# Kernel optimization log

Hardware: AMD Instinct MI355X
Metric: run time of the kernel (lower is better)

Reference implementation:

```python
import jax, jax.numpy as jnp
import numpy as np
import math

K = 30   # neighbors
T = 9    # num_kernel

def sparsemax(z):
    # sparsemax along last axis
    zs = jnp.sort(z, axis=-1)[..., ::-1]
    rng = jnp.arange(1, z.shape[-1] + 1, dtype=z.dtype)
    cs = jnp.cumsum(zs, axis=-1)
    support = (1.0 + rng * zs) > cs
    kz = jnp.sum(support, axis=-1, keepdims=True)
    tau = (jnp.take_along_axis(cs, kz - 1, axis=-1) - 1.0) / kz.astype(z.dtype)
    return jnp.maximum(z - tau, 0.0)

def bn(x, g, b, axes, eps=1e-5):
    # batch-norm (training-mode batch stats), channel axis = 1
    m = jnp.mean(x, axes, keepdims=True)
    v = jnp.var(x, axes, keepdims=True)
    sh = [1] * x.ndim; sh[1] = -1
    return (x - m) / jnp.sqrt(v + eps) * g.reshape(sh) + b.reshape(sh)

def _forward(x, B_ff, mlp_W, permx, W1, b1, S1, W2, b2, S2, W3, b3, S3, W4, b4, S4,
             W5, g5, be5, L1, g6, be6, L2, bL2, g7, be7, L3, bL3):
    Bsz, _, N = x.shape
    pts = jnp.transpose(x, (0, 2, 1))                      # [B,N,3]
    # knn (DGCNN-style): negative squared distance, top-k (self first)
    xx = jnp.sum(pts * pts, -1)                            # [B,N]
    inner = jnp.einsum('bnc,bmc->bnm', pts, pts)
    negd = 2.0 * inner - xx[:, :, None] - xx[:, None, :]
    _, idx = jax.lax.top_k(negd, K)                        # [B,N,K] int32
    gather = jax.vmap(lambda f, i: f[i])                   # [B,N,F],[B,N,K]->[B,N,K,F]
    # Fourier features -> sparsemax basis weights -> per-point permatrix
    ng = gather(pts, idx)                                  # [B,N,K,3]
    xrep = jnp.broadcast_to(ng[:, :, :1, :], ng.shape)     # self repeated
    rel = ng - xrep
    sq = jnp.sum(rel * rel, -1, keepdims=True)
    dist = jnp.where(sq > 0, jnp.sqrt(jnp.where(sq > 0, sq, 1.0)), 0.0)  # safe norm
    feats = jnp.concatenate([xrep, rel, dist], -1).reshape(Bsz, N, 7 * K)
    ff = (2.0 * math.pi) * (feats @ B_ff)                  # [B,N,32]
    ff = jnp.concatenate([jnp.sin(ff), jnp.cos(ff)], -1)   # [B,N,64]
    w = sparsemax(ff @ mlp_W)                              # [B,N,16]
    P = jnp.einsum('bni,ikt->bnkt', w, permx)              # [B,N,K,T]

    def paiconv(f, W, b, S):  # f: [B,Cin,N]
        ft = jnp.transpose(f, (0, 2, 1))                   # [B,N,Cin]
        nb = gather(ft, idx)                               # [B,N,K,Cin]
        agg = jnp.einsum('bnkc,bnkt->bntc', nb, P).reshape(Bsz, N, -1)
        out = agg @ W + b + ft @ S                         # [B,N,Cout]
        return jnp.transpose(out, (0, 2, 1))

    gelu = lambda a: jax.nn.gelu(a, approximate=False)
    x1 = gelu(paiconv(x,  W1, b1, S1))
    x2 = gelu(paiconv(x1, W2, b2, S2))
    x3 = gelu(paiconv(x2, W3, b3, S3))
    x4 = gelu(paiconv(x3, W4, b4, S4))
    f = jnp.concatenate([x1, x2, x3, x4], 1)               # [B,512,N]
    f = jnp.einsum('bcn,ce->ben', f, W5)                   # conv5 (1x1)
    f = gelu(bn(f, g5, be5, (0, 2)))
    h = jnp.concatenate([jnp.max(f, -1), jnp.mean(f, -1)], -1)  # [B,2048]
    h = gelu(bn(h @ L1, g6, be6, (0,)))
    h = gelu(bn(h @ L2 + bL2, g7, be7, (0,)))
    return h @ L3 + bL3


def setup_inputs() -> dict:
    key = jax.random.key(0)
    ks = jax.random.split(key, 20)
    rn = lambda k_, sh, s=1.0: jax.random.normal(k_, sh, dtype=jnp.float32) * s
    B, N = 16, 1024
    inp = {}
    inp['x'] = rn(ks[0], (B, 3, N))
    inp['B_ff'] = rn(ks[1], (7 * K, 32))
    inp['mlp_W'] = rn(ks[2], (64, 16), 0.125)
    inp['permx'] = rn(ks[3], (16, K, T), 0.1)
    dims = [(3, 64), (64, 64), (64, 128), (128, 256)]
    for i, (ci, co) in enumerate(dims, 1):
        inp['W%d' % i] = rn(ks[3 + i], (T * ci, co), 1.0 / float(np.sqrt(T * ci)))
        inp['b%d' % i] = jnp.zeros((co,), jnp.float32)
        inp['S%d' % i] = rn(ks[7 + i], (ci, co), 1.0 / float(np.sqrt(ci)))
    inp['W5'] = rn(ks[12], (512, 1024), 1.0 / float(np.sqrt(512)))
    inp['g5'] = jnp.ones((1024,), jnp.float32); inp['be5'] = jnp.zeros((1024,), jnp.float32)
    inp['L1'] = rn(ks[13], (2048, 512), 1.0 / float(np.sqrt(2048)))
    inp['g6'] = jnp.ones((512,), jnp.float32); inp['be6'] = jnp.zeros((512,), jnp.float32)
    inp['L2'] = rn(ks[14], (512, 256), 1.0 / float(np.sqrt(512))); inp['bL2'] = jnp.zeros((256,), jnp.float32)
    inp['g7'] = jnp.ones((256,), jnp.float32); inp['be7'] = jnp.zeros((256,), jnp.float32)
    inp['L3'] = rn(ks[15], (256, 40), 1.0 / float(np.sqrt(256))); inp['bL3'] = jnp.zeros((40,), jnp.float32)
    return inp


def reference(x, B_ff, mlp_W, permx, W1, b1, S1, W2, b2, S2, W3, b3, S3, W4, b4, S4,
              W5, g5, be5, L1, g6, be6, L2, bL2, g7, be7, L3, bL3):
    return _forward(x, B_ff, mlp_W, permx, W1, b1, S1, W2, b2, S2, W3, b3, S3, W4, b4, S4,
                    W5, g5, be5, L1, g6, be6, L2, bL2, g7, be7, L3, bL3)
```

## Files before the change

kernel.cpp:

```cpp
#include <hip/hip_runtime.h>
#include <hip/hip_bf16.h>
#include <cstddef>

#define BSZ 16
#define NPT 1024
#define KNN 30
#define TKR 9
#define FLT_BIG 3.402823466e+38f

typedef unsigned short u16;
typedef __attribute__((ext_vector_type(8))) u16 u16x8;
typedef __attribute__((ext_vector_type(4))) float f32x4;

__device__ __forceinline__ float gelu_f(float x) {
    return 0.5f * x * (1.0f + erff(x * 0.7071067811865476f));
}

__device__ __forceinline__ u16 bf16_rne(float a) {
    unsigned u = __float_as_uint(a);
    u += 0x7FFFu + ((u >> 16) & 1u);
    return (u16)(u >> 16);
}
__device__ __forceinline__ float bf16_tof(u16 h) {
    return __uint_as_float(((unsigned)h) << 16);
}
__device__ __forceinline__ void split_bf16(float a, u16& h, u16& l) {
    h = bf16_rne(a);
    float r = a - bf16_tof(h);
    l = bf16_rne(r);
}

__device__ __forceinline__ size_t pack_off(int row, int k, int npanels_row) {
    return (size_t)((k >> 5) * npanels_row + (row >> 7)) * 4096
         + (size_t)(((k >> 3) & 3) * 1024 + (row & 127) * 8 + (k & 7));
}

__global__ __launch_bounds__(256) void prep_all(
    const float* __restrict__ x, float* __restrict__ pts,
    const float* __restrict__ W1, const float* __restrict__ S1, float* __restrict__ wz1,
    const float* __restrict__ W2, const float* __restrict__ S2, float* __restrict__ wz2,
    const float* __restrict__ W3, const float* __restrict__ S3, float* __restrict__ wz3,
    const float* __restrict__ W4, const float* __restrict__ S4,
    u16* __restrict__ w4tH, u16* __restrict__ w4tL) {
    int layer = blockIdx.y;
    int t = blockIdx.x * 256 + threadIdx.x;
    if (layer == 0) {
        if (t >= BSZ * NPT) return;
        int b = t >> 10, n = t & 1023;
        const float* xp = x + (size_t)b * 3 * NPT;
        pts[t * 3 + 0] = xp[n];
        pts[t * 3 + 1] = xp[NPT + n];
        pts[t * 3 + 2] = xp[2 * NPT + n];
        return;
    }
    if (layer == 4) {
        if (t >= 1280 * 256) return;
        int k = t >> 8, n = t & 255;
        float v = (k < 1152) ? W4[(size_t)k * 256 + n] : S4[(size_t)(k - 1152) * 256 + n];
        u16 h, l;
        split_bf16(v, h, l);
        size_t off = pack_off(n, k, 2);
        w4tH[off] = h;
        w4tL[off] = l;
        return;
    }
    const float *W, *S; float* WZ; int KW, KS, N, kpad;
    if (layer == 1)      { W = W1; S = S1; WZ = wz1; KW = 27;   KS = 3;   N = 64;  kpad = 32;  }
    else if (layer == 2) { W = W2; S = S2; WZ = wz2; KW = 576;  KS = 64;  N = 64;  kpad = 640; }
    else                 { W = W3; S = S3; WZ = wz3; KW = 576;  KS = 64;  N = 128; kpad = 640; }
    if (t >= kpad * N) return;
    int k = t / N, n = t - k * N;
    float v = 0.0f;
    if (k < KW) v = W[(size_t)k * N + n];
    else if (k < KW + KS) v = S[(size_t)(k - KW) * N + n];
    WZ[t] = v;
}

__global__ __launch_bounds__(256) void knn_basis_kernel(
    const float* __restrict__ pts, const float* __restrict__ B_ff,
    const float* __restrict__ mlp_W, const float* __restrict__ permx,
    int* __restrict__ idx, float* __restrict__ P) {
    __shared__ float npt[4][KNN * 3];
    __shared__ float feats[4][7 * KNN];
    __shared__ float sc[4][64];
    __shared__ float zl[4][16];
    __shared__ float w[4][16];
    __shared__ float sZs[4][16];
    __shared__ float sCs[4][16];
    __shared__ int sIds[4][KNN];
    int tid = threadIdx.x;
    int wave = tid >> 6, lane = tid & 63;
    int bn_ = blockIdx.x * 4 + wave;
    int b = bn_ >> 10;

    {
        double px = (double)pts[(size_t)bn_ * 3 + 0];
        double py = (double)pts[(size_t)bn_ * 3 + 1];
        double pz = (double)pts[(size_t)bn_ * 3 + 2];
        double xn = px * px + py * py + pz * pz;
        const float* pb = pts + (size_t)(b << 10) * 3;
        int base = lane * 16;
        unsigned mono[16];
        #pragma unroll
        for (int j = 0; j < 16; j++) {
            int m = base + j;
            double qx = (double)pb[m * 3 + 0];
            double qy = (double)pb[m * 3 + 1];
            double qz = (double)pb[m * 3 + 2];
            double inner = px * qx + py * qy + pz * qz;
            double xm = qx * qx + qy * qy + qz * qz;
            double cd = 2.0 * inner - xn - xm;
            float cf = (float)cd;
            unsigned bb = __float_as_uint(cf);
            mono[j] = (bb & 0x80000000u) ? ~bb : (bb | 0x80000000u);
        }
        unsigned alive = 0xFFFFu;
        unsigned c1v = 0u, c2v = 0u;
        int c1j = 0, c2j = 0;
        #pragma unroll
        for (int j = 0; j < 16; j++) {
            unsigned v = mono[j];
            if (v > c1v) { c2v = c1v; c2j = c1j; c1v = v; c1j = j; }
            else if (v > c2v) { c2v = v; c2j = j; }
        }
        bool have2 = true;
        for (int it = 0; it < KNN; it++) {
            unsigned m = c1v;
            #pragma unroll
            for (int s = 1; s < 64; s <<= 1) {
                unsigned ov = (unsigned)__shfl_xor((int)m, s, 64);
                m = (ov > m) ? ov : m;
            }
            unsigned long long ball = __ballot(c1v == m);
            int wlan = (int)__builtin_ctzll(ball);
            int jw = __shfl(c1j, wlan, 64);
            int bi = (wlan << 4) + jw;
            if (lane == it) sIds[wave][it] = bi;
            if (lane == wlan) {
                alive &= ~(1u << c1j);
                if (have2) {
                    c1v = c2v; c1j = c2j; have2 = false;
                } else {
                    unsigned a1 = 0u, a2 = 0u;
                    int j1 = 0, j2 = 0;
                    #pragma unroll
                    for (int j = 0; j < 16; j++) {
                        unsigned v = ((alive >> j) & 1u) ? mono[j] : 0u;
                        if (v > a1) { a2 = a1; j2 = j1; a1 = v; j1 = j; }
                        else if (v > a2) { a2 = v; j2 = j; }
                    }
                    c1v = a1; c1j = j1; c2v = a2; c2j = j2;
                    have2 = true;
                }
            }
        }
        __builtin_amdgcn_wave_barrier();
        if (lane < KNN) idx[(size_t)bn_ * KNN + lane] = sIds[wave][lane];
    }
    __syncthreads();

    if (lane < KNN) {
        int m = sIds[wave][lane];
        const float* q = pts + ((size_t)(b << 10) + m) * 3;
        npt[wave][lane * 3 + 0] = q[0];
        npt[wave][lane * 3 + 1] = q[1];
        npt[wave][lane * 3 + 2] = q[2];
    }
    __syncthreads();
    if (lane < KNN) {
        float sx = npt[wave][0], sy = npt[wave][1], sz = npt[wave][2];
        float rx = npt[wave][lane * 3 + 0] - sx;
        float ry = npt[wave][lane * 3 + 1] - sy;
        float rz = npt[wave][lane * 3 + 2] - sz;
        float sq = rx * rx + ry * ry + rz * rz;
        float dist = (sq > 0.0f) ? sqrtf(sq) : 0.0f;
        feats[wave][lane * 7 + 0] = sx;
        feats[wave][lane * 7 + 1] = sy;
        feats[wave][lane * 7 + 2] = sz;
        feats[wave][lane * 7 + 3] = rx;
        feats[wave][lane * 7 + 4] = ry;
        feats[wave][lane * 7 + 5] = rz;
        feats[wave][lane * 7 + 6] = dist;
    }
    __syncthreads();
    {
        int j = lane & 31;
        int half = lane >> 5;
        int i0 = half * 105;
        float acc = 0.0f;
        for (int i = i0; i < i0 + 105; i++) acc += feats[wave][i] * B_ff[i * 32 + j];
        acc += __shfl_xor(acc, 32, 64);
        if (half == 0) {
            float ffv = 6.283185307179586f * acc;
            sc[wave][j] = sinf(ffv);
            sc[wave][j + 32] = cosf(ffv);
        }
    }
    __syncthreads();
    {
        int j = lane & 15;
        int h = lane >> 4;
        float acc = 0.0f;
        for (int i = 16 * h; i < 16 * h + 16; i++) acc += sc[wave][i] * mlp_W[i * 16 + j];
        acc += __shfl_xor(acc, 16, 64);
        acc += __shfl_xor(acc, 32, 64);
        if (h == 0) zl[wave][j] = acc;
    }
    __syncthreads();
    {
        int l = lane & 15;
        float zv = zl[wave][l];
        int rank = 0;
        #pragma unroll
        for (int j = 0; j < 16; j++) {
            float zj = zl[wave][j];
            rank += (zj > zv || (zj == zv && j < l)) ? 1 : 0;
        }
        if (lane < 16) sZs[wave][rank] = zv;
        __builtin_amdgcn_wave_barrier();
        float cs = 0.0f;
        #pragma unroll
        for (int p = 0; p < 16; p++) {
            float zp = sZs[wave][p];
            cs += (p <= l) ? zp : 0.0f;
        }
        float zsl = sZs[wave][l];
        bool flag = (lane < 16) && (1.0f + (float)(l + 1) * zsl > cs);
        unsigned long long ball = __ballot(flag);
        int cnt = (int)__popcll(ball & 0xFFFFull);
        if (lane < 16) sCs[wave][l] = cs;
        __builtin_amdgcn_wave_barrier();
        float tau = (sCs[wave][cnt - 1] - 1.0f) / (float)cnt;
        if (lane < 16) w[wave][l] = fmaxf(zv - tau, 0.0f);
    }
    __syncthreads();
    float* Pp = P + (size_t)bn_ * (KNN * TKR);
    for (int e = lane; e < KNN * TKR; e += 64) {
        int k = e / TKR, t = e - TKR * k;
        float acc = 0.0f;
        for (int i = 0; i < 16; i++) acc += w[wave][i] * permx[(i * KNN + k) * TKR + t];
        Pp[e] = acc;
    }
}

template <int CIN>
__global__ __launch_bounds__(256) void agg_kernel(
    const float* __restrict__ ft, int ftst,
    const float* __restrict__ P, const int* __restrict__ idx,
    float* __restrict__ Z, int kpad) {
    __shared__ float sP[KNN * TKR];
    __shared__ float sNb[KNN * CIN];
    __shared__ int sIdx[KNN];
    int bn_ = blockIdx.x;
    int b = bn_ >> 10;
    int tid = threadIdx.x;
    if (tid < KNN) sIdx[tid] = idx[(size_t)bn_ * KNN + tid];
    for (int e = tid; e < KNN * TKR; e += 256) sP[e] = P[(size_t)bn_ * (KNN * TKR) + e];
    __syncthreads();
    for (int e = tid; e < KNN * CIN; e += 256) {
        int k = e / CIN, c = e - k * CIN;
        sNb[e] = ft[((size_t)(b << 10) + sIdx[k]) * ftst + c];
    }
    __syncthreads();
    float* zp = Z + (size_t)bn_ * kpad;
    const int KW = TKR * CIN;
    for (int e = tid; e < kpad; e += 256) {
        float v;
        if (e < KW) {
            int t = e / CIN, c = e - t * CIN;
            float acc = 0.0f;
            #pragma unroll
            for (int k = 0; k < KNN; k++) acc += sNb[k * CIN + c] * sP[k * TKR + t];
            v = acc;
        } else if (e < KW + CIN) {
            v = ft[(size_t)bn_ * ftst + (e - KW)];
        } else {
            v = 0.0f;
        }
        zp[e] = v;
    }
}

template <int CIN>
__global__ __launch_bounds__(256) void agg_v_kernel(
    const float* __restrict__ ft, int ftst,
    const float* __restrict__ P, const int* __restrict__ idx,
    float* __restrict__ Z, int kpad) {
    __shared__ float sP[KNN * TKR];
    __shared__ float sNb[KNN * CIN];
    __shared__ int sIdx[KNN];
    constexpr int C4 = CIN / 4;
    int bn_ = blockIdx.x;
    int b = bn_ >> 10;
    int tid = threadIdx.x;
    if (tid < KNN) sIdx[tid] = idx[(size_t)bn_ * KNN + tid];
    for (int e = tid; e < KNN * TKR; e += 256) sP[e] = P[(size_t)bn_ * (KNN * TKR) + e];
    __syncthreads();
    for (int e = tid; e < KNN * C4; e += 256) {
        int k = e / C4, c4 = (e - k * C4) * 4;
        *(float4*)&sNb[k * CIN + c4] =
            *(const float4*)&ft[((size_t)(b << 10) + sIdx[k]) * ftst + c4];
    }
    __syncthreads();
    float* zp = Z + (size_t)bn_ * kpad;
    const int KW = TKR * CIN;
    for (int e = tid; e < (kpad >> 2); e += 256) {
        int c0 = e * 4;
        float4 v;
        if (c0 < KW) {
            int t = c0 / CIN, c4 = c0 - t * CIN;
            float4 a = make_float4(0.f, 0.f, 0.f, 0.f);
            #pragma unroll
            for (int k = 0; k < KNN; k++) {
                float p = sP[k * TKR + t];
                float4 nb = *(const float4*)&sNb[k * CIN + c4];
                a.x += nb.x * p; a.y += nb.y * p;
                a.z += nb.z * p; a.w += nb.w * p;
            }
            v = a;
        } else if (c0 < KW + CIN) {
            v = *(const float4*)&ft[(size_t)bn_ * ftst + (c0 - KW)];
        } else {
            v = make_float4(0.f, 0.f, 0.f, 0.f);
        }
        *(float4*)&zp[c0] = v;
    }
}

template <int CIN>
__global__ __launch_bounds__(256) void agg_v_split_kernel(
    const float* __restrict__ ft, int ftst,
    const float* __restrict__ P, const int* __restrict__ idx,
    u16* __restrict__ ZH, u16* __restrict__ ZL, int kpad) {
    __shared__ float sP[KNN * TKR];
    __shared__ float sNb[KNN * CIN];
    __shared__ int sIdx[KNN];
    constexpr int C4 = CIN / 4;
    int bn_ = blockIdx.x;
    int b = bn_ >> 10;
    int tid = threadIdx.x;
    if (tid < KNN) sIdx[tid] = idx[(size_t)bn_ * KNN + tid];
    for (int e = tid; e < KNN * TKR; e += 256) sP[e] = P[(size_t)bn_ * (KNN * TKR) + e];
    __syncthreads();
    for (int e = tid; e < KNN * C4; e += 256) {
        int k = e / C4, c4 = (e - k * C4) * 4;
        *(float4*)&sNb[k * CIN + c4] =
            *(const float4*)&ft[((size_t)(b << 10) + sIdx[k]) * ftst + c4];
    }
    __syncthreads();
    const int KW = TKR * CIN;
    for (int e = tid; e < (kpad >> 2); e += 256) {
        int c0 = e * 4;
        float4 v;
        if (c0 < KW) {
            int t = c0 / CIN, c4 = c0 - t * CIN;
            float4 a = make_float4(0.f, 0.f, 0.f, 0.f);
            #pragma unroll
            for (int k = 0; k < KNN; k++) {
                float p = sP[k * TKR + t];
                float4 nb = *(const float4*)&sNb[k * CIN + c4];
                a.x += nb.x * p; a.y += nb.y * p;
                a.z += nb.z * p; a.w += nb.w * p;
            }
            v = a;
        } else if (c0 < KW + CIN) {
            v = *(const float4*)&ft[(size_t)bn_ * ftst + (c0 - KW)];
        } else {
            v = make_float4(0.f, 0.f, 0.f, 0.f);
        }
        u16 h[4], l[4];
        split_bf16(v.x, h[0], l[0]);
        split_bf16(v.y, h[1], l[1]);
        split_bf16(v.z, h[2], l[2]);
        split_bf16(v.w, h[3], l[3]);
        uint2 hv, lv;
        hv.x = (unsigned)h[0] | ((unsigned)h[1] << 16);
        hv.y = (unsigned)h[2] | ((unsigned)h[3] << 16);
        lv.x = (unsigned)l[0] | ((unsigned)l[1] << 16);
        lv.y = (unsigned)l[2] | ((unsigned)l[3] << 16);
        size_t off = pack_off(bn_, c0, 128);
        *(uint2*)&ZH[off] = hv;
        *(uint2*)&ZL[off] = lv;
    }
}

template <bool GELU, bool HASBIAS>
__global__ __launch_bounds__(256) void gemm_f32_64db(
    const float* __restrict__ A, int lda,
    const float* __restrict__ B, int ldb, int K,
    const float* __restrict__ bias,
    float* __restrict__ C, int ldc) {
    __shared__ float As[2][16][64];
    __shared__ float Bs[2][16][64];
    int tid = threadIdx.x;
    int tx = tid & 15, ty = tid >> 4;
    int m0 = blockIdx.y * 64, n0 = blockIdx.x * 64;
    float acc[4][4];
    #pragma unroll
    for (int i = 0; i < 4; i++)
        #pragma unroll
        for (int j = 0; j < 4; j++) acc[i][j] = 0.0f;

    int ar = tid >> 2, ac0 = (tid & 3) * 4;
    const float* aptr = A + (size_t)(m0 + ar) * lda + ac0;
    int br = tid >> 4, bc = (tid & 15) * 4;
    const float* bptr = B + (size_t)br * ldb + n0 + bc;

    float4 pa = *(const float4*)(aptr);
    float4 pb = *(const float4*)(bptr);
    As[0][ac0 + 0][ar] = pa.x; As[0][ac0 + 1][ar] = pa.y;
    As[0][ac0 + 2][ar] = pa.z; As[0][ac0 + 3][ar] = pa.w;
    *(float4*)&Bs[0][br][bc] = pb;
    __syncthreads();

    int nk = K >> 4;
    for (int t = 0; t < nk; t++) {
        int buf = t & 1;
        bool more = (t + 1) < nk;
        if (more) {
            int k0 = (t + 1) << 4;
            pa = *(const float4*)(aptr + k0);
            pb = *(const float4*)(bptr + (size_t)k0 * ldb);
        }
        #pragma unroll
        for (int kk = 0; kk < 16; kk++) {
            float av[4], bv[4];
            *(float4*)&av[0] = *(const float4*)&As[buf][kk][ty * 4];
            *(float4*)&bv[0] = *(const float4*)&Bs[buf][kk][tx * 4];
            #pragma unroll
            for (int i = 0; i < 4; i++)
                #pragma unroll
                for (int j = 0; j < 4; j++) acc[i][j] += av[i] * bv[j];
        }
        if (more) {
            int nb = 1 - buf;
            As[nb][ac0 + 0][ar] = pa.x; As[nb][ac0 + 1][ar] = pa.y;
            As[nb][ac0 + 2][ar] = pa.z; As[nb][ac0 + 3][ar] = pa.w;
            *(float4*)&Bs[nb][br][bc] = pb;
        }
        __syncthreads();
    }
    #pragma unroll
    for (int i = 0; i < 4; i++) {
        int r = m0 + ty * 4 + i;
        int c = n0 + tx * 4;
        float v[4];
        #pragma unroll
        for (int j = 0; j < 4; j++) {
            float t = acc[i][j];
            if (HASBIAS) t += bias[c + j];
            if (GELU) t = gelu_f(t);
            v[j] = t;
        }
        *(float4*)(C + (size_t)r * ldc + c) = *(float4*)v;
    }
}

__global__ __launch_bounds__(256) void convert_split(
    const float* __restrict__ feat, u16* __restrict__ fH, u16* __restrict__ fL,
    const float* __restrict__ W5, u16* __restrict__ wH, u16* __restrict__ wL) {
    int t = blockIdx.x * 256 + threadIdx.x;
    if (blockIdx.y == 0) {
        int base = t << 3;
        int row = base >> 9, k0 = base & 511;
        float4 a = *(const float4*)&feat[base];
        float4 b = *(const float4*)&feat[base + 4];
        float v[8] = {a.x, a.y, a.z, a.w, b.x, b.y, b.z, b.w};
        u16 h[8], l[8];
        #pragma unroll
        for (int i = 0; i < 8; i++) split_bf16(v[i], h[i], l[i]);
        uint4 hv, lv;
        hv.x = (unsigned)h[0] | ((unsigned)h[1] << 16);
        hv.y = (unsigned)h[2] | ((unsigned)h[3] << 16);
        hv.z = (unsigned)h[4] | ((unsigned)h[5] << 16);
        hv.w = (unsigned)h[6] | ((unsigned)h[7] << 16);
        lv.x = (unsigned)l[0] | ((unsigned)l[1] << 16);
        lv.y = (unsigned)l[2] | ((unsigned)l[3] << 16);
        lv.z = (unsigned)l[4] | ((unsigned)l[5] << 16);
        lv.w = (unsigned)l[6] | ((unsigned)l[7] << 16);
        size_t off = pack_off(row, k0, 128);
        *(uint4*)&fH[off] = hv;
        *(uint4*)&fL[off] = lv;
    } else {
        if (t >= 512 * 1024) return;
        int n = t >> 9, k = t & 511;
        u16 h, l;
        split_bf16(W5[(size_t)k * 1024 + n], h, l);
        size_t off = pack_off(n, k, 8);
        wH[off] = h; wL[off] = l;
    }
}

template <bool STATS, bool GELU, bool HASBIAS>
__global__ __launch_bounds__(256) void mfma_bf16x3(
    const u16* __restrict__ fH, const u16* __restrict__ fL,
    const u16* __restrict__ wH, const u16* __restrict__ wL,
    int K, const float* __restrict__ bias,
    float* __restrict__ C, int ldc,
    float* __restrict__ partS, float* __restrict__ partQ) {
    __shared__ __align__(16) u16 lds[2][16384];
    int tid = threadIdx.x;
    int lane = tid & 63, wave = tid >> 6;
    int wr = wave >> 1, wc = wave & 1;
    int kg = lane >> 4, r = lane & 15;

    int nwg = gridDim.x * gridDim.y;
    int hw = blockIdx.y * gridDim.x + blockIdx.x;
    int logical = (hw & 7) * (nwg >> 3) + (hw >> 3);
    int nb = logical % gridDim.x;
    int mb = logical / gridDim.x;
    int m0 = mb << 7, n0 = nb << 7;
    int nmp = gridDim.y;
    int nnp = gridDim.x;

    const u16* src = (wave == 0) ? fH : (wave == 1) ? fL
                   : (wave == 2) ? wH : wL;

    f32x4 acc[4][4];
    #pragma unroll
    for (int i = 0; i < 4; i++)
        #pragma unroll
        for (int j = 0; j < 4; j++) {
            acc[i][j][0] = 0.0f; acc[i][j][1] = 0.0f;
            acc[i][j][2] = 0.0f; acc[i][j][3] = 0.0f;
        }

#define STAGE_K(BUF, TT) {                                                     \
    size_t tb = ((size_t)((wave < 2) ? ((TT) * nmp + mb)                       \
                                     : ((TT) * nnp + nb)) << 12);              \
    _Pragma("unroll")                                                          \
    for (int iw = 0; iw < 8; iw++) {                                           \
        const u16* gp = src + tb + (size_t)(((iw << 6) + lane) << 3);          \
        __builtin_amdgcn_global_load_lds(                                      \
            (const __attribute__((address_space(1))) void*)gp,                 \
            (__attribute__((address_space(3))) void*)&lds[BUF][(wave << 12) + (iw << 9)], \
            16, 0, 0);                                                         \
    } }

    int nk = K >> 5;
    STAGE_K(0, 0);
    __syncthreads();
    for (int t = 0; t < nk; t++) {
        if (t + 1 < nk) STAGE_K((t + 1) & 1, (t + 1));
        const u16* lb = lds[t & 1];
        u16x8 bh[4], bl[4];
        #pragma unroll
        for (int fj = 0; fj < 4; fj++) {
            int bcol = (wc << 6) + (fj << 4) + r;
            bh[fj] = *(const u16x8*)&lb[ 8192 + (((kg << 7) + bcol) << 3)];
            bl[fj] = *(const u16x8*)&lb[12288 + (((kg << 7) + bcol) << 3)];
        }
        #pragma unroll
        for (int fi = 0; fi < 4; fi++) {
            int arow = (wr << 6) + (fi << 4) + r;
            u16x8 ah = *(const u16x8*)&lb[       (((kg << 7) + arow) << 3)];
            u16x8 al = *(const u16x8*)&lb[4096 + (((kg << 7) + arow) << 3)];
            #pragma unroll
            for (int fj = 0; fj < 4; fj++) {
                asm volatile("v_mfma_f32_16x16x32_bf16 %0, %1, %2, %0"
                             : "+v"(acc[fi][fj]) : "v"(ah), "v"(bh[fj]));
                asm volatile("v_mfma_f32_16x16x32_bf16 %0, %1, %2, %0"
                             : "+v"(acc[fi][fj]) : "v"(ah), "v"(bl[fj]));
                asm volatile("v_mfma_f32_16x16x32_bf16 %0, %1, %2, %0"
                             : "+v"(acc[fi][fj]) : "v"(al), "v"(bh[fj]));
            }
        }
        __syncthreads();
    }
#undef STAGE_K

    asm volatile("s_nop 15\n\ts_nop 15" ::: "memory");

    float bvv[4];
    if (HASBIAS) {
        #pragma unroll
        for (int fj = 0; fj < 4; fj++) bvv[fj] = bias[n0 + (wc << 6) + (fj << 4) + r];
    }

    #pragma unroll
    for (int fi = 0; fi < 4; fi++)
        #pragma unroll
        for (int ri = 0; ri < 4; ri++) {
            int row = m0 + (wr << 6) + (fi << 4) + (kg << 2) + ri;
            float* cp = C + (size_t)row * ldc + n0 + (wc << 6) + r;
            #pragma unroll
            for (int fj = 0; fj < 4; fj++) {
                float v = acc[fi][fj][ri];
                if (HASBIAS) v += bvv[fj];
                if (GELU) v = gelu_f(v);
                cp[fj << 4] = v;
            }
        }

    if (STATS) {
        __syncthreads();
        float* sS = (float*)lds;
        float* sQ = sS + 1024;
        int slot = (wr << 2) + kg;
        #pragma unroll
        for (int fj = 0; fj < 4; fj++) {
            float s = 0.0f, q = 0.0f;
            #pragma unroll
            for (int fi = 0; fi < 4; fi++)
                #pragma unroll
                for (int ri = 0; ri < 4; ri++) {
                    float v = acc[fi][fj][ri];
                    s += v; q += v * v;
                }
            int cl = (wc << 6) + (fj << 4) + r;
            sS[slot * 128 + cl] = s;
            sQ[slot * 128 + cl] = q;
        }
        __syncthreads();
        if (tid < 128) {
            float S = 0.0f, Q = 0.0f;
            #pragma unroll
            for (int i = 0; i < 8; i++) { S += sS[i * 128 + tid]; Q += sQ[i * 128 + tid]; }
            partS[(size_t)mb * 1024 + n0 + tid] = S;
            partQ[(size_t)mb * 1024 + n0 + tid] = Q;
        }
    }
}

__global__ __launch_bounds__(256) void stats_reduce(
    const float* __restrict__ partS, const float* __restrict__ partQ,
    const float* __restrict__ g, const float* __restrict__ be,
    float* __restrict__ scaleb, float* __restrict__ shiftb) {
    int e = blockIdx.x * 256 + threadIdx.x;
    if (e >= 1024) return;
    double s = 0.0, q = 0.0;
    for (int mb = 0; mb < 128; mb++) {
        s += (double)partS[(size_t)mb * 1024 + e];
        q += (double)partQ[(size_t)mb * 1024 + e];
    }
    double m = s * (1.0 / 16384.0);
    double v = q * (1.0 / 16384.0) - m * m;
    float sc = g[e] * (float)(1.0 / sqrt(v + 1e-5));
    scaleb[e] = sc;
    shiftb[e] = be[e] - (float)m * sc;
}

__global__ __launch_bounds__(256) void pool_partial(
    const float* __restrict__ f5, const float* __restrict__ scaleb,
    const float* __restrict__ shiftb,
    float* __restrict__ partM, double* __restrict__ partSd) {
    int chunk = blockIdx.x, g = blockIdx.y, b = blockIdx.z;
    int tid = threadIdx.x;
    int lane = tid & 63, nlane = tid >> 6;
    int c0 = (g << 8) + lane * 4;
    float4 sc = *(const float4*)&scaleb[c0];
    float4 sh = *(const float4*)&shiftb[c0];
    float m0 = -FLT_BIG, m1 = -FLT_BIG, m2 = -FLT_BIG, m3 = -FLT_BIG;
    double s0 = 0.0, s1 = 0.0, s2 = 0.0, s3 = 0.0;
    int nend = (chunk + 1) << 6;
    for (int n = (chunk << 6) + nlane; n < nend; n += 4) {
        float4 v = *(const float4*)&f5[((size_t)(b << 10) + n) * 1024 + c0];
        float g0 = gelu_f(v.x * sc.x + sh.x);
        float g1 = gelu_f(v.y * sc.y + sh.y);
        float g2 = gelu_f(v.z * sc.z + sh.z);
        float g3 = gelu_f(v.w * sc.w + sh.w);
        m0 = fmaxf(m0, g0); m1 = fmaxf(m1, g1);
        m2 = fmaxf(m2, g2); m3 = fmaxf(m3, g3);
        s0 += (double)g0; s1 += (double)g1;
        s2 += (double)g2; s3 += (double)g3;
    }
    __shared__ float smax[4][256];
    __shared__ double ssum[4][256];
    *(float4*)&smax[nlane][lane * 4] = make_float4(m0, m1, m2, m3);
    ssum[nlane][lane * 4 + 0] = s0;
    ssum[nlane][lane * 4 + 1] = s1;
    ssum[nlane][lane * 4 + 2] = s2;
    ssum[nlane][lane * 4 + 3] = s3;
    __syncthreads();
    if (nlane == 0) {
        size_t base = ((size_t)((b * 4 + g) * 16 + chunk)) * 256 + lane * 4;
        #pragma unroll
        for (int j = 0; j < 4; j++) {
            float mm = smax[0][lane * 4 + j];
            double ss = ssum[0][lane * 4 + j];
            #pragma unroll
            for (int i = 1; i < 4; i++) {
                mm = fmaxf(mm, smax[i][lane * 4 + j]);
                ss += ssum[i][lane * 4 + j];
            }
            partM[base + j] = mm;
            partSd[base + j] = ss;
        }
    }
}

__global__ __launch_bounds__(256) void pool_finish(
    const float* __restrict__ partM, const double* __restrict__ partSd,
    float* __restrict__ h) {
    int b = blockIdx.x;
    int e0 = threadIdx.x * 4;
    int g = e0 >> 8, cl = e0 & 255;
    float mm[4] = {-FLT_BIG, -FLT_BIG, -FLT_BIG, -FLT_BIG};
    double ss[4] = {0.0, 0.0, 0.0, 0.0};
    for (int chunk = 0; chunk < 16; chunk++) {
        size_t base = ((size_t)((b * 4 + g) * 16 + chunk)) * 256 + cl;
        float4 pm = *(const float4*)&partM[base];
        mm[0] = fmaxf(mm[0], pm.x); mm[1] = fmaxf(mm[1], pm.y);
        mm[2] = fmaxf(mm[2], pm.z); mm[3] = fmaxf(mm[3], pm.w);
        ss[0] += partSd[base + 0]; ss[1] += partSd[base + 1];
        ss[2] += partSd[base + 2]; ss[3] += partSd[base + 3];
    }
    #pragma unroll
    for (int j = 0; j < 4; j++) {
        h[(size_t)b * 2048 + e0 + j] = mm[j];
        h[(size_t)b * 2048 + 1024 + e0 + j] = (float)(ss[j] * (1.0 / 1024.0));
    }
}

__global__ __launch_bounds__(256) void fc_split(
    const float* __restrict__ X, const float* __restrict__ W,
    double* __restrict__ part, int Bn, int In, int Out, int KC) {
    int tid = blockIdx.x * 256 + threadIdx.x;
    if (tid >= Bn * Out * KC) return;
    int chunk = tid / (Bn * Out);
    int r = tid - chunk * (Bn * Out);
    int b = r / Out, j = r - b * Out;
    int len = In / KC;
    int i0 = chunk * len;
    const float* x = X + (size_t)b * In + i0;
    const float* w = W + (size_t)i0 * Out + j;
    double acc = 0.0;
    for (int i = 0; i < len; i++) acc += (double)x[i] * (double)w[(size_t)i * Out];
    part[tid] = acc;
}

__global__ __launch_bounds__(256) void fc_bn_gelu(
    const double* __restrict__ part, const float* __restrict__ bias,
    const float* __restrict__ g, const float* __restrict__ be,
    float* __restrict__ Y, int Out, int KC) {
    int j = blockIdx.x * 256 + threadIdx.x;
    if (j >= Out) return;
    float r[BSZ];
    for (int b = 0; b < BSZ; b++) {
        double acc = bias ? (double)bias[j] : 0.0;
        for (int c = 0; c < KC; c++) acc += part[(size_t)c * (BSZ * Out) + b * Out + j];
        r[b] = (float)acc;
    }
    double m = 0.0;
    for (int b = 0; b < BSZ; b++) m += (double)r[b];
    m /= (double)BSZ;
    double v = 0.0;
    for (int b = 0; b < BSZ; b++) {
        double dd = (double)r[b] - m;
        v += dd * dd;
    }
    v /= (double)BSZ;
    float sc = g[j] * (float)(1.0 / sqrt(v + 1e-5));
    float sh = be[j] - (float)m * sc;
    for (int b = 0; b < BSZ; b++) Y[b * Out + j] = gelu_f(r[b] * sc + sh);
}

__global__ __launch_bounds__(256) void fc_reduce(
    const double* __restrict__ part, const float* __restrict__ bias,
    float* __restrict__ Y, int Bn, int Out, int KC) {
    int r = blockIdx.x * 256 + threadIdx.x;
    if (r >= Bn * Out) return;
    int j = r % Out;
    double acc = bias ? (double)bias[j] : 0.0;
    for (int c = 0; c < KC; c++) acc += part[(size_t)c * (Bn * Out) + r];
    Y[r] = (float)acc;
}

extern "C" void kernel_launch(void* const* d_in, const int* in_sizes, int n_in,
                              void* d_out, int out_size, void* d_ws, size_t ws_size,
                              hipStream_t stream) {
    const float* x     = (const float*)d_in[0];
    const float* B_ff  = (const float*)d_in[1];
    const float* mlp_W = (const float*)d_in[2];
    const float* permx = (const float*)d_in[3];
    const float* W1 = (const float*)d_in[4];
    const float* b1 = (const float*)d_in[5];
    const float* S1 = (const float*)d_in[6];
    const float* W2 = (const float*)d_in[7];
    const float* b2 = (const float*)d_in[8];
    const float* S2 = (const float*)d_in[9];
    const float* W3 = (const float*)d_in[10];
    const float* b3 = (const float*)d_in[11];
    const float* S3 = (const float*)d_in[12];
    const float* W4 = (const float*)d_in[13];
    const float* b4 = (const float*)d_in[14];
    const float* S4 = (const float*)d_in[15];
    const float* W5 = (const float*)d_in[16];
    const float* g5 = (const float*)d_in[17];
    const float* be5 = (const float*)d_in[18];
    const float* L1 = (const float*)d_in[19];
    const float* g6 = (const float*)d_in[20];
    const float* be6 = (const float*)d_in[21];
    const float* L2 = (const float*)d_in[22];
    const float* bL2 = (const float*)d_in[23];
    const float* g7 = (const float*)d_in[24];
    const float* be7 = (const float*)d_in[25];
    const float* L3 = (const float*)d_in[26];
    const float* bL3 = (const float*)d_in[27];
    float* outp = (float*)d_out;

    const int BN = BSZ * NPT;

    float* ws = (float*)d_ws;
    float* pts   = ws;
    int*   idxb  = (int*)(ws + 49152);
    float* Pb    = ws + 540672;
    float* feat  = Pb + 4423680;
    float* Zbig  = feat + 8388608;
    u16*   ZH    = (u16*)Zbig;
    u16*   ZL    = (u16*)(Zbig + 10485760);
    float* f5    = Zbig;
    u16*   featH = (u16*)(Zbig + 16777216);
    float* poolM = Zbig + 16777216;
    double* poolS = (double*)(Zbig + 16777216 + 262144);
    float* w4slot = Zbig + 20971520;
    u16*   w4tH  = (u16*)w4slot;
    u16*   w4tL  = w4tH + 327680;
    float* scb   = w4slot + 327680;
    float* shb   = scb + 1024;
    float* hb    = shb + 1024;
    float* y1    = hb + 32768;
    float* y2    = y1 + 8192;
    float* partC_S = y2 + 4096;
    float* partC_Q = partC_S + 131072;
    double* partF  = (double*)(partC_Q + 131072);
    float* wsend = (float*)(partF + 131072);
    u16* featL = (u16*)ws;
    u16* w5tH  = (u16*)(ws + 4194304);
    u16* w5tL  = (u16*)(ws + 4456448);
    float* wz1   = Zbig + 11010048;
    float* wz2   = wz1 + 2048;
    float* wz3   = wz2 + 40960;
    size_t need_bytes = (size_t)(wsend - ws) * sizeof(float);
    if (ws_size < need_bytes) return;

    prep_all<<<dim3(1280, 5), 256, 0, stream>>>(
        x, pts, W1, S1, wz1, W2, S2, wz2, W3, S3, wz3, W4, S4, w4tH, w4tL);

    knn_basis_kernel<<<BN / 4, 256, 0, stream>>>(pts, B_ff, mlp_W, permx, idxb, Pb);

    agg_kernel<3><<<BN, 256, 0, stream>>>(pts, 3, Pb, idxb, Zbig, 32);
    gemm_f32_64db<true, true><<<dim3(1, 256), 256, 0, stream>>>(
        Zbig, 32, wz1, 64, 32, b1, feat + 0, 512);
    agg_v_kernel<64><<<BN, 256, 0, stream>>>(feat + 0, 512, Pb, idxb, Zbig, 640);
    gemm_f32_64db<true, true><<<dim3(1, 256), 256, 0, stream>>>(
        Zbig, 640, wz2, 64, 640, b2, feat + 64, 512);
    agg_v_kernel<64><<<BN, 256, 0, stream>>>(feat + 64, 512, Pb, idxb, Zbig, 640);
    gemm_f32_64db<true, true><<<dim3(2, 256), 256, 0, stream>>>(
        Zbig, 640, wz3, 128, 640, b3, feat + 128, 512);
    agg_v_split_kernel<128><<<BN, 256, 0, stream>>>(feat + 128, 512, Pb, idxb, ZH, ZL, 1280);
    mfma_bf16x3<false, true, true><<<dim3(2, 128), 256, 0, stream>>>(
        ZH, ZL, w4tH, w4tL, 1280, b4, feat + 256, 512, nullptr, nullptr);

    convert_split<<<dim3(4096, 2), 256, 0, stream>>>(feat, featH, featL, W5, w5tH, w5tL);
    mfma_bf16x3<true, false, false><<<dim3(8, 128), 256, 0, stream>>>(
        featH, featL, w5tH, w5tL, 512, nullptr, f5, 1024, partC_S, partC_Q);

    stats_reduce<<<4, 256, 0, stream>>>(partC_S, partC_Q, g5, be5, scb, shb);
    pool_partial<<<dim3(16, 4, BSZ), 256, 0, stream>>>(f5, scb, shb, poolM, poolS);
    pool_finish<<<BSZ, 256, 0, stream>>>(poolM, poolS, hb);

    fc_split<<<(BSZ * 512 * 16 + 255) / 256, 256, 0, stream>>>(hb, L1, partF, BSZ, 2048, 512, 16);
    fc_bn_gelu<<<2, 256, 0, stream>>>(partF, nullptr, g6, be6, y1, 512, 16);
    fc_split<<<(BSZ * 256 * 8 + 255) / 256, 256, 0, stream>>>(y1, L2, partF, BSZ, 512, 256, 8);
    fc_bn_gelu<<<1, 256, 0, stream>>>(partF, bL2, g7, be7, y2, 256, 8);
    fc_split<<<(BSZ * 40 * 4 + 255) / 256, 256, 0, stream>>>(y2, L3, partF, BSZ, 256, 40, 4);
    fc_reduce<<<(BSZ * 40 + 255) / 256, 256, 0, stream>>>(partF, bL3, outp, BSZ, 40, 4);
}
```

Measured before the change: 743.0 us.

## Process four points per block in split aggregation and coalesce packed bf16 writes

The split aggregation kernel now handles four points per block, one per wavefront. Outputs are staged in shared memory and then written out in the packed tile layout, so each store covers contiguous runs across rows instead of scattered 8-byte writes. The feature-conversion kernel remaps its thread indices the same way, so consecutive threads write consecutive packed offsets. This uses more shared memory per block, which may lower occupancy, and it hardcodes the packed layout arithmetic.

```diff
diff --git a/kernel.cpp b/kernel.cpp
--- a/kernel.cpp
+++ b/kernel.cpp
@@ -327,60 +327,86 @@
     }
 }
 
-template <int CIN>
-__global__ __launch_bounds__(256) void agg_v_split_kernel(
+__global__ __launch_bounds__(256) void agg_v_split4_kernel(
     const float* __restrict__ ft, int ftst,
     const float* __restrict__ P, const int* __restrict__ idx,
-    u16* __restrict__ ZH, u16* __restrict__ ZL, int kpad) {
-    __shared__ float sP[KNN * TKR];
-    __shared__ float sNb[KNN * CIN];
-    __shared__ int sIdx[KNN];
-    constexpr int C4 = CIN / 4;
-    int bn_ = blockIdx.x;
-    int b = bn_ >> 10;
+    u16* __restrict__ ZH, u16* __restrict__ ZL) {
+    __shared__ int   sIdx4[4][KNN];
+    __shared__ float sP4[4][KNN * TKR + 2];
+    __shared__ float sNb4[4][KNN * 128];
+    __shared__ __align__(16) u16 oH[4][640];
+    __shared__ __align__(16) u16 oL[4][640];
     int tid = threadIdx.x;
-    if (tid < KNN) sIdx[tid] = idx[(size_t)bn_ * KNN + tid];
-    for (int e = tid; e < KNN * TKR; e += 256) sP[e] = P[(size_t)bn_ * (KNN * TKR) + e];
-    __syncthreads();
-    for (int e = tid; e < KNN * C4; e += 256) {
-        int k = e / C4, c4 = (e - k * C4) * 4;
-        *(float4*)&sNb[k * CIN + c4] =
-            *(const float4*)&ft[((size_t)(b << 10) + sIdx[k]) * ftst + c4];
-    }
-    __syncthreads();
-    const int KW = TKR * CIN;
-    for (int e = tid; e < (kpad >> 2); e += 256) {
-        int c0 = e * 4;
-        float4 v;
-        if (c0 < KW) {
-            int t = c0 / CIN, c4 = c0 - t * CIN;
-            float4 a = make_float4(0.f, 0.f, 0.f, 0.f);
-            #pragma unroll
-            for (int k = 0; k < KNN; k++) {
-                float p = sP[k * TKR + t];
-                float4 nb = *(const float4*)&sNb[k * CIN + c4];
-                a.x += nb.x * p; a.y += nb.y * p;
-                a.z += nb.z * p; a.w += nb.w * p;
+    int wave = tid >> 6, lane = tid & 63;
+    int r0 = blockIdx.x << 2;
+    int b = r0 >> 10;
+    const int KW = TKR * 128;
+
+    if (tid < 4 * KNN) {
+        int row = tid / KNN, k = tid - row * KNN;
+        sIdx4[row][k] = idx[(size_t)(r0 + row) * KNN + k];
+    }
+    for (int e = tid; e < 4 * KNN * TKR; e += 256) {
+        int row = e / (KNN * TKR), i = e - row * (KNN * TKR);
+        sP4[row][i] = P[(size_t)(r0 + row) * (KNN * TKR) + i];
+    }
+    __syncthreads();
+    for (int e = tid; e < 4 * KNN * 32; e += 256) {
+        int row = e / (KNN * 32), rem = e - row * (KNN * 32);
+        int k = rem >> 5, c4 = (rem & 31) << 2;
+        *(float4*)&sNb4[row][k * 128 + c4] =
+            *(const float4*)&ft[((size_t)(b << 10) + sIdx4[row][k]) * ftst + c4];
+    }
+    __syncthreads();
+
+    #pragma unroll
+    for (int pass = 0; pass < 2; pass++) {
+        int ebase = pass * 640;
+        for (int q = lane; q < 160; q += 64) {
+            int e0 = ebase + q * 4;
+            float4 v;
+            if (e0 < KW) {
+                int t = e0 >> 7, c = e0 & 127;
+                float4 a = make_float4(0.f, 0.f, 0.f, 0.f);
+                #pragma unroll
+                for (int k = 0; k < KNN; k++) {
+                    float p = sP4[wave][k * TKR + t];
+                    float4 nb = *(const float4*)&sNb4[wave][k * 128 + c];
+                    a.x += nb.x * p; a.y += nb.y * p;
+                    a.z += nb.z * p; a.w += nb.w * p;
+                }
+                v = a;
+            } else if (e0 < KW + 128) {
+                v = *(const float4*)&ft[(size_t)(r0 + wave) * ftst + (e0 - KW)];
+            } else {
+                v = make_float4(0.f, 0.f, 0.f, 0.f);
             }
-            v = a;
-        } else if (c0 < KW + CIN) {
-            v = *(const float4*)&ft[(size_t)bn_ * ftst + (c0 - KW)];
-        } else {
-            v = make_float4(0.f, 0.f, 0.f, 0.f);
-        }
-        u16 h[4], l[4];
-        split_bf16(v.x, h[0], l[0]);
-        split_bf16(v.y, h[1], l[1]);
-        split_bf16(v.z, h[2], l[2]);
-        split_bf16(v.w, h[3], l[3]);
-        uint2 hv, lv;
-        hv.x = (unsigned)h[0] | ((unsigned)h[1] << 16);
-        hv.y = (unsigned)h[2] | ((unsigned)h[3] << 16);
-        lv.x = (unsigned)l[0] | ((unsigned)l[1] << 16);
-        lv.y = (unsigned)l[2] | ((unsigned)l[3] << 16);
-        size_t off = pack_off(bn_, c0, 128);
-        *(uint2*)&ZH[off] = hv;
-        *(uint2*)&ZL[off] = lv;
+            u16 h[4], l[4];
+            split_bf16(v.x, h[0], l[0]);
+            split_bf16(v.y, h[1], l[1]);
+            split_bf16(v.z, h[2], l[2]);
+            split_bf16(v.w, h[3], l[3]);
+            uint2 hv, lv;
+            hv.x = (unsigned)h[0] | ((unsigned)h[1] << 16);
+            hv.y = (unsigned)h[2] | ((unsigned)h[3] << 16);
+            lv.x = (unsigned)l[0] | ((unsigned)l[1] << 16);
+            lv.y = (unsigned)l[2] | ((unsigned)l[3] << 16);
+            *(uint2*)&oH[wave][q * 4] = hv;
+            *(uint2*)&oL[wave][q * 4] = lv;
+        }
+        __syncthreads();
+        for (int u = tid; u < 640; u += 256) {
+            int kpl = u >> 5, s = u & 31;
+            int kc = s >> 3, row = (s >> 1) & 3, half = s & 1;
+            int eloc = kpl * 32 + kc * 8 + half * 4;
+            uint2 hv = *(const uint2*)&oH[row][eloc];
+            uint2 lv = *(const uint2*)&oL[row][eloc];
+            size_t off = (size_t)((pass * 20 + kpl) * 128 + (r0 >> 7)) * 4096
+                       + (size_t)(kc * 1024 + ((r0 & 127) + row) * 8 + half * 4);
+            *(uint2*)&ZH[off] = hv;
+            *(uint2*)&ZL[off] = lv;
+        }
+        __syncthreads();
     }
 }
 
@@ -461,10 +487,14 @@
     const float* __restrict__ W5, u16* __restrict__ wH, u16* __restrict__ wL) {
     int t = blockIdx.x * 256 + threadIdx.x;
     if (blockIdx.y == 0) {
-        int base = t << 3;
-        int row = base >> 9, k0 = base & 511;
-        float4 a = *(const float4*)&feat[base];
-        float4 b = *(const float4*)&feat[base + 4];
+        int T = t >> 9, s = t & 511;
+        int kc = s >> 7, rloc = s & 127;
+        int kp = T >> 7, rp = T & 127;
+        int row = (rp << 7) + rloc;
+        int k0 = (kp << 5) + (kc << 3);
+        const float* fp = &feat[(size_t)row * 512 + k0];
+        float4 a = *(const float4*)fp;
+        float4 b = *(const float4*)(fp + 4);
         float v[8] = {a.x, a.y, a.z, a.w, b.x, b.y, b.z, b.w};
         u16 h[8], l[8];
         #pragma unroll
@@ -478,7 +508,7 @@
         lv.y = (unsigned)l[2] | ((unsigned)l[3] << 16);
         lv.z = (unsigned)l[4] | ((unsigned)l[5] << 16);
         lv.w = (unsigned)l[6] | ((unsigned)l[7] << 16);
-        size_t off = pack_off(row, k0, 128);
+        size_t off = (size_t)T * 4096 + kc * 1024 + rloc * 8;
         *(uint4*)&fH[off] = hv;
         *(uint4*)&fL[off] = lv;
     } else {
@@ -848,7 +878,7 @@
     agg_v_kernel<64><<<BN, 256, 0, stream>>>(feat + 64, 512, Pb, idxb, Zbig, 640);
     gemm_f32_64db<true, true><<<dim3(2, 256), 256, 0, stream>>>(
         Zbig, 640, wz3, 128, 640, b3, feat + 128, 512);
-    agg_v_split_kernel<128><<<BN, 256, 0, stream>>>(feat + 128, 512, Pb, idxb, ZH, ZL, 1280);
+    agg_v_split4_kernel<<<BN / 4, 256, 0, stream>>>(feat + 128, 512, Pb, idxb, ZH, ZL);
     mfma_bf16x3<false, true, true><<<dim3(2, 128), 256, 0, stream>>>(
         ZH, ZL, w4tH, w4tL, 1280, b4, feat + 256, 512, nullptr, nullptr);
 
```

Measured after the change: 788.7 us. +6.2%, slower.
